# Optimization experiments

Hardware: AMD Instinct MI355X
Metric: run time of the kernel (lower is better)

The kernel has to match this reference:

```python
import jax, jax.numpy as jnp
import numpy as np

GAP = 1.0
THRESHOLD = 0.1


def setup_inputs() -> dict:
    key = jax.random.key(0)
    k1, k2 = jax.random.split(key)
    B = 8192
    return {
        "input": jax.random.normal(k1, (B, 1), dtype=jnp.float32),
        "gdt_ts": jax.random.uniform(k2, (B,), dtype=jnp.float32),
    }


def reference(input, gdt_ts):
    # o: [B] predicted scores
    o = jnp.squeeze(input)
    B = o.shape[0]
    # pairwise label differences [B, B]
    ld = gdt_ts[:, None] - gdt_ts[None, :]
    # y_ij = -1 if tm_i < tm_j else +1 (ties -> +1, matching torch code)
    y = jnp.where(ld < 0, -1.0, 1.0).astype(o.dtype)
    # example weight: 1 if |tm_i - tm_j| > threshold else 0
    # (diagonal has ld == 0 so weight 0 -> i == j pairs drop out automatically)
    w = (jnp.abs(ld) > THRESHOLD).astype(o.dtype)
    # hinge: max(0, gap + y_ij * (o_i - o_j))
    hinge = jnp.maximum(0.0, GAP + y * (o[:, None] - o[None, :]))
    N = B * (B - 1)  # number of ordered i != j pairs
    loss = jnp.sum(w * hinge) / N
    return loss[None]  # shape [1], matching the torch module
```

## Files before the change

kernel.cpp:

```cpp
#include <hip/hip_runtime.h>


constexpr int BLOCK  = 256;
constexpr int TILE_I = 4;
constexpr int JCHUNK = 64;
constexpr float GAP = 1.0f;
constexpr float THRESHOLD = 0.1f;

__global__ __launch_bounds__(BLOCK) void pair_loss_kernel(
        const float* __restrict__ o, const float* __restrict__ t,
        float* __restrict__ partials) {
    __shared__ float so[JCHUNK];
    __shared__ float st[JCHUNK];

    const int tid = threadIdx.x;
    const int j0  = blockIdx.y * JCHUNK;

    if (tid < JCHUNK)                 so[tid] = o[j0 + tid];
    else if (tid < 2 * JCHUNK)        st[tid - JCHUNK] = t[j0 + tid - JCHUNK];
    __syncthreads();

    const int ibase = blockIdx.x * (BLOCK * TILE_I) + tid;
    float oi[TILE_I], ti[TILE_I];
#pragma unroll
    for (int k = 0; k < TILE_I; ++k) {
        oi[k] = o[ibase + k * BLOCK];
        ti[k] = t[ibase + k * BLOCK];
    }

    float acc[TILE_I] = {0.f, 0.f, 0.f, 0.f};
#pragma unroll 8
    for (int j = 0; j < JCHUNK; ++j) {
        const float oj = so[j];
        const float tj = st[j];
#pragma unroll
        for (int k = 0; k < TILE_I; ++k) {
            const float ld   = ti[k] - tj;
            const float diff = oi[k] - oj;
            const unsigned sgn = __float_as_uint(ld) & 0x80000000u;
            const float yd  = __uint_as_float(__float_as_uint(diff) ^ sgn);
            const float s   = GAP + yd;
            acc[k] += (fabsf(ld) > THRESHOLD) ? fmaxf(s, 0.0f) : 0.0f;
        }
    }

    float a = (acc[0] + acc[1]) + (acc[2] + acc[3]);
    for (int off = 32; off > 0; off >>= 1)
        a += __shfl_down(a, off, 64);

    __shared__ float wsum[BLOCK / 64];
    if ((tid & 63) == 0) wsum[tid >> 6] = a;
    __syncthreads();

    if (tid == 0) {
        float s = 0.0f;
#pragma unroll
        for (int w = 0; w < BLOCK / 64; ++w) s += wsum[w];
        partials[blockIdx.y * gridDim.x + blockIdx.x] = s;
    }
}

__global__ __launch_bounds__(BLOCK) void reduce_kernel(
        const float* __restrict__ partials, float* __restrict__ out,
        int nblk, int B) {
    const int tid = threadIdx.x;
    float a = 0.0f;
    for (int p = tid; p < nblk; p += BLOCK) a += partials[p];

    for (int off = 32; off > 0; off >>= 1)
        a += __shfl_down(a, off, 64);

    __shared__ float wsum[BLOCK / 64];
    if ((tid & 63) == 0) wsum[tid >> 6] = a;
    __syncthreads();

    if (tid == 0) {
        float s = 0.0f;
#pragma unroll
        for (int w = 0; w < BLOCK / 64; ++w) s += wsum[w];
        const float N = (float)((long long)B * (long long)(B - 1));
        out[0] = s / N;
    }
}

extern "C" void kernel_launch(void* const* d_in, const int* in_sizes, int n_in,
                              void* d_out, int out_size, void* d_ws, size_t ws_size,
                              hipStream_t stream) {
    const float* o = (const float*)d_in[0];
    const float* t = (const float*)d_in[1];
    float* out = (float*)d_out;
    float* ws  = (float*)d_ws;

    const int B = in_sizes[1];

    dim3 grid(B / (BLOCK * TILE_I), B / JCHUNK);
    pair_loss_kernel<<<grid, BLOCK, 0, stream>>>(o, t, ws);

    const int nblk = grid.x * grid.y;
    reduce_kernel<<<1, BLOCK, 0, stream>>>(ws, out, nblk, B);
}
```

Baseline: 69.37 us.

## Exploit pairwise symmetry to compute only the lower triangle and double it

The weighted hinge term is symmetric in (i, j), so the kernel now evaluates only pairs with j < i and the reduction multiplies the sum by two. Blocks entirely above the diagonal write a zero partial and exit early. Diagonal blocks apply a per-element j < i mask, and the j chunk is halved so the triangle boundary is cut more finely. The shared-memory staging of the j values is replaced by direct uniform global loads. This roughly halves the pairwise arithmetic, at the cost of load imbalance across blocks, twice as many blocks, and extra masking on the diagonal tiles.

```diff
diff --git a/kernel.cpp b/kernel.cpp
--- a/kernel.cpp
+++ b/kernel.cpp
@@ -3,24 +3,25 @@
 
 constexpr int BLOCK  = 256;
 constexpr int TILE_I = 4;
-constexpr int JCHUNK = 64;
+constexpr int ITILE  = BLOCK * TILE_I;
+constexpr int JCHUNK = 32;
 constexpr float GAP = 1.0f;
 constexpr float THRESHOLD = 0.1f;
 
 __global__ __launch_bounds__(BLOCK) void pair_loss_kernel(
         const float* __restrict__ o, const float* __restrict__ t,
         float* __restrict__ partials) {
-    __shared__ float so[JCHUNK];
-    __shared__ float st[JCHUNK];
+    const int tid  = threadIdx.x;
+    const int i_lo = blockIdx.x * ITILE;
+    const int j0   = blockIdx.y * JCHUNK;
+    const int pidx = blockIdx.y * gridDim.x + blockIdx.x;
 
-    const int tid = threadIdx.x;
-    const int j0  = blockIdx.y * JCHUNK;
+    if (j0 >= i_lo + ITILE) {
+        if (tid == 0) partials[pidx] = 0.0f;
+        return;
+    }
 
-    if (tid < JCHUNK)                 so[tid] = o[j0 + tid];
-    else if (tid < 2 * JCHUNK)        st[tid - JCHUNK] = t[j0 + tid - JCHUNK];
-    __syncthreads();
-
-    const int ibase = blockIdx.x * (BLOCK * TILE_I) + tid;
+    const int ibase = i_lo + tid;
     float oi[TILE_I], ti[TILE_I];
 #pragma unroll
     for (int k = 0; k < TILE_I; ++k) {
@@ -29,18 +30,39 @@
     }
 
     float acc[TILE_I] = {0.f, 0.f, 0.f, 0.f};
+
+    if (j0 < i_lo) {
 #pragma unroll 8
-    for (int j = 0; j < JCHUNK; ++j) {
-        const float oj = so[j];
-        const float tj = st[j];
+        for (int j = 0; j < JCHUNK; ++j) {
+            const float oj = o[j0 + j];
+            const float tj = t[j0 + j];
 #pragma unroll
-        for (int k = 0; k < TILE_I; ++k) {
-            const float ld   = ti[k] - tj;
-            const float diff = oi[k] - oj;
-            const unsigned sgn = __float_as_uint(ld) & 0x80000000u;
-            const float yd  = __uint_as_float(__float_as_uint(diff) ^ sgn);
-            const float s   = GAP + yd;
-            acc[k] += (fabsf(ld) > THRESHOLD) ? fmaxf(s, 0.0f) : 0.0f;
+            for (int k = 0; k < TILE_I; ++k) {
+                const float ld   = ti[k] - tj;
+                const float diff = oi[k] - oj;
+                const unsigned sgn = __float_as_uint(ld) & 0x80000000u;
+                const float yd = __uint_as_float(__float_as_uint(diff) ^ sgn);
+                const float s  = GAP + yd;
+                acc[k] += (fabsf(ld) > THRESHOLD) ? fmaxf(s, 0.0f) : 0.0f;
+            }
+        }
+    } else {
+#pragma unroll 8
+        for (int j = 0; j < JCHUNK; ++j) {
+            const int   jg = j0 + j;
+            const float oj = o[jg];
+            const float tj = t[jg];
+#pragma unroll
+            for (int k = 0; k < TILE_I; ++k) {
+                const int ig = ibase + k * BLOCK;
+                const float ld   = ti[k] - tj;
+                const float diff = oi[k] - oj;
+                const unsigned sgn = __float_as_uint(ld) & 0x80000000u;
+                const float yd = __uint_as_float(__float_as_uint(diff) ^ sgn);
+                const float s  = GAP + yd;
+                const bool  w  = (fabsf(ld) > THRESHOLD) && (jg < ig);
+                acc[k] += w ? fmaxf(s, 0.0f) : 0.0f;
+            }
         }
     }
 
@@ -56,7 +78,7 @@
         float s = 0.0f;
 #pragma unroll
         for (int w = 0; w < BLOCK / 64; ++w) s += wsum[w];
-        partials[blockIdx.y * gridDim.x + blockIdx.x] = s;
+        partials[pidx] = s;
     }
 }
 
@@ -79,7 +101,7 @@
 #pragma unroll
         for (int w = 0; w < BLOCK / 64; ++w) s += wsum[w];
         const float N = (float)((long long)B * (long long)(B - 1));
-        out[0] = s / N;
+        out[0] = 2.0f * s / N;
     }
 }
 
@@ -93,7 +115,7 @@
 
     const int B = in_sizes[1];
 
-    dim3 grid(B / (BLOCK * TILE_I), B / JCHUNK);
+    dim3 grid(B / ITILE, B / JCHUNK);
     pair_loss_kernel<<<grid, BLOCK, 0, stream>>>(o, t, ws);
 
     const int nblk = grid.x * grid.y;
```

New measurement: 72.80 us. 1.05x slower.
